# Kernel tuning notes

Hardware: AMD Instinct MI355X
Metric: run time of the kernel (lower is better)

## Reference

```python
import jax, jax.numpy as jnp
import numpy as np

B, T, D = 32, 512, 256
F = 256  # duration_predictor_filter_size
K = 3    # kernel size, padding=1
MEL_MAX = 2304
EPS = 1e-5


def _conv1d(x, w, b):
    # x: [B, T, C_in], w: [C_out, C_in, K], 'same'-ish padding=1
    y = jax.lax.conv_general_dilated(
        x.transpose(0, 2, 1), w, window_strides=(1,), padding=[(1, 1)],
        dimension_numbers=("NCH", "OIH", "NCH"))
    return y.transpose(0, 2, 1) + b


def _layernorm(x, g, b):
    mu = jnp.mean(x, axis=-1, keepdims=True)
    var = jnp.mean(jnp.square(x - mu), axis=-1, keepdims=True)
    return (x - mu) * jax.lax.rsqrt(var + EPS) * g + b


def setup_inputs() -> dict:
    key = jax.random.key(0)
    ks = jax.random.split(key, 8)
    x = jax.random.normal(ks[0], (B, T, D), dtype=jnp.float32)
    target = jax.random.randint(ks[1], (B, T), 0, 8, dtype=jnp.int32)
    s = 0.02
    return {
        "x": x,
        "target": target,
        "mel_max_length": MEL_MAX,
        "conv1_w": jax.random.normal(ks[2], (F, D, K), dtype=jnp.float32) * s,
        "conv1_b": jnp.zeros((F,), jnp.float32),
        "ln1_g": jnp.ones((F,), jnp.float32),
        "ln1_b": jnp.zeros((F,), jnp.float32),
        "conv2_w": jax.random.normal(ks[3], (F, F, K), dtype=jnp.float32) * s,
        "conv2_b": jnp.zeros((F,), jnp.float32),
        "ln2_g": jnp.ones((F,), jnp.float32),
        "ln2_b": jnp.zeros((F,), jnp.float32),
        "lin_w": jax.random.normal(ks[4], (1, F), dtype=jnp.float32) * s,
        "lin_b": jnp.zeros((1,), jnp.float32),
    }


def reference(x, target, mel_max_length, conv1_w, conv1_b, ln1_g, ln1_b,
              conv2_w, conv2_b, ln2_g, ln2_b, lin_w, lin_b):
    # Variance_adaptor (duration predictor), eval-mode dropout = identity
    h = jax.nn.relu(_layernorm(_conv1d(x, conv1_w, conv1_b), ln1_g, ln1_b))
    h = jax.nn.relu(_layernorm(_conv1d(h, conv2_w, conv2_b), ln2_g, ln2_b))
    dur_pred = jax.nn.relu(jnp.einsum("btf,of->bto", h, lin_w) + lin_b)[..., 0]  # [B,T]

    # LR: alignment @ x, expressed as the equivalent duration-indexed gather.
    # alignment[b, t_out, j] = 1 iff cumsum(dur)[b,j-1] <= t_out < cumsum(dur)[b,j]
    cum = jnp.cumsum(target, axis=1)                    # [B, T]
    t_out = jnp.arange(mel_max_length, dtype=cum.dtype)  # [T_out]
    idx = jax.vmap(lambda c: jnp.searchsorted(c, t_out, side="right"))(cum)  # [B, T_out]
    valid = (t_out[None, :] < cum[:, -1:]).astype(x.dtype)                   # [B, T_out]
    gathered = jnp.take_along_axis(x, jnp.clip(idx, 0, T - 1)[:, :, None], axis=1)
    output = gathered * valid[:, :, None]                # zeros past total length (pad)
    return output, dur_pred
```

## Files before the change

### kernel.cpp

```cpp
#include <hip/hip_runtime.h>

typedef __attribute__((ext_vector_type(8))) short short8;
typedef __attribute__((ext_vector_type(4))) float floatx4;

typedef __attribute__((address_space(3))) unsigned int lds_u32;
typedef __attribute__((address_space(1))) const unsigned int glb_u32;

static __device__ __forceinline__ unsigned short f2bf(float f) {
    unsigned int u = __float_as_uint(f);
    return (unsigned short)((u + 0x7FFFu + ((u >> 16) & 1u)) >> 16);
}
static __device__ __forceinline__ void cp16(const ushort* g, ushort* l) {
    __builtin_amdgcn_global_load_lds((glb_u32*)g, (lds_u32*)l, 16, 0, 0);
}

__global__ __launch_bounds__(256)
void prep_kernel(const float* __restrict__ x, const int* __restrict__ target,
                 const float* __restrict__ w1, const float* __restrict__ w2,
                 ushort* __restrict__ xb, ushort* __restrict__ h1b,
                 ushort* __restrict__ w1q, ushort* __restrict__ w2q,
                 float* __restrict__ out0)
{
    __shared__ int cum[512], ps[256], sidx[64];
    const int blk = blockIdx.x, tid = threadIdx.x;
    if (blk < 1152) {
        const int b = blk / 36, t0o = (blk % 36) * 64;
        const int v0 = target[b * 512 + 2 * tid];
        const int v1 = target[b * 512 + 2 * tid + 1];
        ps[tid] = v0 + v1;
        __syncthreads();
        for (int off = 1; off < 256; off <<= 1) {
            int t = (tid >= off) ? ps[tid - off] : 0;
            __syncthreads();
            ps[tid] += t;
            __syncthreads();
        }
        const int excl = tid ? ps[tid - 1] : 0;
        cum[2 * tid]     = excl + v0;
        cum[2 * tid + 1] = excl + v0 + v1;
        __syncthreads();
        const int total = cum[511];
        if (tid < 64) {
            int t = t0o + tid;
            int lo = 0, hi = 512;
            while (lo < hi) {
                int mid = (lo + hi) >> 1;
                if (cum[mid] <= t) lo = mid + 1; else hi = mid;
            }
            sidx[tid] = (t < total) ? ((lo < 512) ? lo : 511) : -1;
        }
        __syncthreads();
        const float4* x4 = (const float4*)x;
        float4* o4 = (float4*)out0;
        const int lane6 = tid & 63, g4 = tid >> 6;
        #pragma unroll 4
        for (int rr = 0; rr < 16; ++rr) {
            int r = rr * 4 + g4;
            int idx = sidx[r];
            float4 v = make_float4(0.f, 0.f, 0.f, 0.f);
            if (idx >= 0) v = x4[((size_t)(b * 512 + idx)) * 64 + lane6];
            o4[((size_t)(b * 2304 + t0o + r)) * 64 + lane6] = v;
        }
    } else if (blk < 5264) {
        const int r = (blk - 1152) * 4 + (tid >> 6);
        const int c = (tid & 63) * 4;
        const int b = r / 514, tp = r % 514;
        ushort4 o;
        if (tp >= 1 && tp <= 512) {
            float4 v = *(const float4*)(x + ((size_t)(b * 512 + tp - 1) * 256 + c));
            o.x = f2bf(v.x); o.y = f2bf(v.y); o.z = f2bf(v.z); o.w = f2bf(v.w);
        } else {
            o.x = o.y = o.z = o.w = 0;
            *(ushort4*)(h1b + (size_t)r * 256 + c) = o;
        }
        *(ushort4*)(xb + (size_t)r * 256 + c) = o;
    } else {
        const bool second = blk >= 6032;
        const int e = (blk - (second ? 6032 : 5264)) * 256 + tid;
        const float* w = second ? w2 : w1;
        ushort* wq = second ? w2q : w1q;
        const int f = e / 768, j = e % 768;
        const int c = j & 255, kr = j >> 8;
        const int se = kr * 4 + (c >> 6);
        const int kk = c & 63;
        const int wg = f >> 6, ni = (f >> 4) & 3, colf = f & 15;
        const int kh = kk >> 5, qk = (kk >> 3) & 3, jj = kk & 7;
        wq[(size_t)se * 16384 + wg * 4096 + (ni * 2 + kh) * 512
           + (qk * 16 + colf) * 8 + jj] = f2bf(w[f * 768 + c * 3 + kr]);
    }
}

template<bool IS_CONV2>
__global__ __launch_bounds__(256, 3)
void conv_mfma_kernel(const ushort* __restrict__ src,
                      const ushort* __restrict__ wq,
                      const float* __restrict__ cbias,
                      const float* __restrict__ gamma, const float* __restrict__ beta,
                      const float* __restrict__ lw, const float* __restrict__ lb,
                      ushort* __restrict__ outb,
                      float* __restrict__ durp)
{
    __shared__ ushort As[2][2048];
    __shared__ float sum_s[4][32], sq_s[4][32], mu_s[32], rs_s[32];

    const int tid = threadIdx.x;
    const int w_ = tid >> 6, lane = tid & 63;
    const int q = lane >> 4, col = lane & 15;
    const int b  = blockIdx.x & 31;
    const int t0 = (blockIdx.x >> 5) << 5;
    const int rot = blockIdx.x % 12;

    floatx4 acc[2][4] = {};
    const int arow = tid >> 3, aquad = (tid & 7) ^ (arow & 7);
    const ushort* xbb = src + (size_t)b * 514 * 256;
    const ushort* bptr = wq + (size_t)w_ * 4096 + lane * 8;

    auto se_of = [&](int s) { int v = s + rot; return v >= 12 ? v - 12 : v; };
#define STAGE_A(SE_, BUF_) do {                                                   \
        const int se_ = (SE_);                                                    \
        const int krow_ = se_ >> 2, cbo_ = (se_ & 3) << 6;                        \
        cp16(xbb + (size_t)(t0 + krow_ + arow) * 256 + cbo_ + aquad * 8,          \
             &As[BUF_][0] + w_ * 512);                                            \
    } while (0)

    STAGE_A(se_of(0), 0);
    __syncthreads();

    int cur = 0;
    #pragma unroll
    for (int s = 0; s < 12; ++s) {
        const int nb = cur ^ 1;
        if (s + 1 < 12) STAGE_A(se_of(s + 1), nb);
        const int se = se_of(s);
        short8 bf[4][2], af[2][2];
        #pragma unroll
        for (int ni = 0; ni < 4; ++ni)
            #pragma unroll
            for (int kh = 0; kh < 2; ++kh)
                bf[ni][kh] = *(const short8*)(bptr + (size_t)se * 16384 + (ni * 2 + kh) * 512);
        #pragma unroll
        for (int mi = 0; mi < 2; ++mi)
            #pragma unroll
            for (int kh = 0; kh < 2; ++kh)
                af[mi][kh] = *(const short8*)((const char*)&As[cur][0]
                    + (mi * 16 + col) * 128 + (((kh * 4 + q) ^ (col & 7)) * 16));
        #pragma unroll
        for (int kh = 0; kh < 2; ++kh)
            #pragma unroll
            for (int mi = 0; mi < 2; ++mi)
                #pragma unroll
                for (int ni = 0; ni < 4; ++ni)
                    acc[mi][ni] = __builtin_amdgcn_mfma_f32_16x16x32_bf16(
                        af[mi][kh], bf[ni][kh], acc[mi][ni], 0, 0, 0);
        __syncthreads();
        cur = nb;
    }
#undef STAGE_A

    const int base_c = w_ * 64;
    float cb4[4], gm4[4], bt4[4];
    #pragma unroll
    for (int ni = 0; ni < 4; ++ni) {
        cb4[ni] = cbias[base_c + ni * 16 + col];
        gm4[ni] = gamma[base_c + ni * 16 + col];
        bt4[ni] = beta [base_c + ni * 16 + col];
    }
    float rsum[2][4] = {}, rsq[2][4] = {};
    #pragma unroll
    for (int mi = 0; mi < 2; ++mi)
        #pragma unroll
        for (int ni = 0; ni < 4; ++ni)
            #pragma unroll
            for (int r = 0; r < 4; ++r) {
                float v = acc[mi][ni][r] + cb4[ni];
                acc[mi][ni][r] = v;
                rsum[mi][r] += v;
                rsq [mi][r] += v * v;
            }
    #pragma unroll
    for (int mi = 0; mi < 2; ++mi)
        #pragma unroll
        for (int r = 0; r < 4; ++r) {
            float s = rsum[mi][r], ss = rsq[mi][r];
            #pragma unroll
            for (int d = 8; d > 0; d >>= 1) {
                s  += __shfl_down(s,  d, 16);
                ss += __shfl_down(ss, d, 16);
            }
            if (col == 0) {
                sum_s[w_][mi * 16 + q * 4 + r] = s;
                sq_s [w_][mi * 16 + q * 4 + r] = ss;
            }
        }
    __syncthreads();
    if (tid < 32) {
        float s  = sum_s[0][tid] + sum_s[1][tid] + sum_s[2][tid] + sum_s[3][tid];
        float ss = sq_s [0][tid] + sq_s [1][tid] + sq_s [2][tid] + sq_s [3][tid];
        float mu = s * (1.f / 256.f);
        mu_s[tid] = mu;
        rs_s[tid] = rsqrtf(ss * (1.f / 256.f) - mu * mu + 1e-5f);
    }
    __syncthreads();

    if (!IS_CONV2) {
        #pragma unroll
        for (int mi = 0; mi < 2; ++mi)
            #pragma unroll
            for (int ni = 0; ni < 4; ++ni)
                #pragma unroll
                for (int r = 0; r < 4; ++r) {
                    int row = mi * 16 + q * 4 + r;
                    float v = (acc[mi][ni][r] - mu_s[row]) * rs_s[row] * gm4[ni] + bt4[ni];
                    outb[((size_t)b * 514 + t0 + row + 1) * 256 + base_c + ni * 16 + col]
                        = f2bf(fmaxf(v, 0.f));
                }
    } else {
        float lw4[4];
        #pragma unroll
        for (int ni = 0; ni < 4; ++ni) lw4[ni] = lw[base_c + ni * 16 + col];
        float dsum[2][4] = {};
        #pragma unroll
        for (int mi = 0; mi < 2; ++mi)
            #pragma unroll
            for (int ni = 0; ni < 4; ++ni)
                #pragma unroll
                for (int r = 0; r < 4; ++r) {
                    int row = mi * 16 + q * 4 + r;
                    float v = (acc[mi][ni][r] - mu_s[row]) * rs_s[row] * gm4[ni] + bt4[ni];
                    dsum[mi][r] += fmaxf(v, 0.f) * lw4[ni];
                }
        #pragma unroll
        for (int mi = 0; mi < 2; ++mi)
            #pragma unroll
            for (int r = 0; r < 4; ++r) {
                float s = dsum[mi][r];
                #pragma unroll
                for (int d = 8; d > 0; d >>= 1) s += __shfl_down(s, d, 16);
                if (col == 0) sum_s[w_][mi * 16 + q * 4 + r] = s;
            }
        __syncthreads();
        if (tid < 32)
            durp[b * 512 + t0 + tid] = fmaxf(sum_s[0][tid] + sum_s[1][tid]
                                           + sum_s[2][tid] + sum_s[3][tid] + lb[0], 0.f);
    }
}

extern "C" void kernel_launch(void* const* d_in, const int* in_sizes, int n_in,
                              void* d_out, int out_size, void* d_ws, size_t ws_size,
                              hipStream_t stream) {
    const float* x      = (const float*)d_in[0];
    const int*   target = (const int*)  d_in[1];
    const float* c1w = (const float*)d_in[3];
    const float* c1b = (const float*)d_in[4];
    const float* g1  = (const float*)d_in[5];
    const float* b1  = (const float*)d_in[6];
    const float* c2w = (const float*)d_in[7];
    const float* c2b = (const float*)d_in[8];
    const float* g2  = (const float*)d_in[9];
    const float* b2  = (const float*)d_in[10];
    const float* lw  = (const float*)d_in[11];
    const float* lb  = (const float*)d_in[12];

    const size_t PADEL = (size_t)32 * 514 * 256;
    ushort* xb   = (ushort*)d_ws;
    ushort* h1b  = xb + PADEL;
    ushort* w1q  = h1b + PADEL;
    ushort* w2q  = w1q + 196608;

    float* out0 = (float*)d_out;
    float* durp = out0 + (size_t)32 * 2304 * 256;

    prep_kernel<<<6800, 256, 0, stream>>>(x, target, c1w, c2w, xb, h1b, w1q, w2q, out0);
    conv_mfma_kernel<false><<<512, 256, 0, stream>>>(
        xb, w1q, c1b, g1, b1, nullptr, nullptr, h1b, nullptr);
    conv_mfma_kernel<true><<<512, 256, 0, stream>>>(
        h1b, w2q, c2b, g2, b2, lw, lb, nullptr, durp);
}
```

Measured before the change: 149.6 us.

## Interleave length-regulator gather blocks into the conv kernels

Moves the length-regulator gather (cumsum, searchsorted, row copy to the output) out of the prep kernel and spreads its 1152 blocks across the two conv launches. Each launch interleaves 8 conv blocks with 9 gather blocks per group of 17, so the memory-bound copy runs alongside the MFMA-bound conv work. The aim is to hide the large output write behind compute and shorten the prep kernel. The cost is higher LDS use per conv block for the extra shared arrays, which may lower occupancy, and blocks within one launch now have uneven work.

```diff
diff --git a/kernel.cpp b/kernel.cpp
--- a/kernel.cpp
+++ b/kernel.cpp
@@ -15,16 +15,65 @@
 }
 
 __global__ __launch_bounds__(256)
-void prep_kernel(const float* __restrict__ x, const int* __restrict__ target,
+void prep_kernel(const float* __restrict__ x,
                  const float* __restrict__ w1, const float* __restrict__ w2,
                  ushort* __restrict__ xb, ushort* __restrict__ h1b,
-                 ushort* __restrict__ w1q, ushort* __restrict__ w2q,
-                 float* __restrict__ out0)
+                 ushort* __restrict__ w1q, ushort* __restrict__ w2q)
 {
+    const int blk = blockIdx.x, tid = threadIdx.x;
+    if (blk < 4112) {
+        const int r = blk * 4 + (tid >> 6);
+        const int c = (tid & 63) * 4;
+        const int b = r / 514, tp = r % 514;
+        ushort4 o;
+        if (tp >= 1 && tp <= 512) {
+            float4 v = *(const float4*)(x + ((size_t)(b * 512 + tp - 1) * 256 + c));
+            o.x = f2bf(v.x); o.y = f2bf(v.y); o.z = f2bf(v.z); o.w = f2bf(v.w);
+        } else {
+            o.x = o.y = o.z = o.w = 0;
+            *(ushort4*)(h1b + (size_t)r * 256 + c) = o;
+        }
+        *(ushort4*)(xb + (size_t)r * 256 + c) = o;
+    } else {
+        const bool second = blk >= 4880;
+        const int e = (blk - (second ? 4880 : 4112)) * 256 + tid;
+        const float* w = second ? w2 : w1;
+        ushort* wq = second ? w2q : w1q;
+        const int f = e / 768, j = e % 768;
+        const int c = j & 255, kr = j >> 8;
+        const int se = kr * 4 + (c >> 6);
+        const int kk = c & 63;
+        const int wg = f >> 6, ni = (f >> 4) & 3, colf = f & 15;
+        const int kh = kk >> 5, qk = (kk >> 3) & 3, jj = kk & 7;
+        wq[(size_t)se * 16384 + wg * 4096 + (ni * 2 + kh) * 512
+           + (qk * 16 + colf) * 8 + jj] = f2bf(w[f * 768 + c * 3 + kr]);
+    }
+}
+
+template<bool IS_CONV2>
+__global__ __launch_bounds__(256, 3)
+void conv_mfma_kernel(const ushort* __restrict__ src,
+                      const ushort* __restrict__ wq,
+                      const float* __restrict__ cbias,
+                      const float* __restrict__ gamma, const float* __restrict__ beta,
+                      const float* __restrict__ lw, const float* __restrict__ lb,
+                      ushort* __restrict__ outb,
+                      float* __restrict__ durp,
+                      const float* __restrict__ x,
+                      const int* __restrict__ target,
+                      float* __restrict__ out0,
+                      int gbase)
+{
+    __shared__ ushort As[2][2048];
+    __shared__ float sum_s[4][32], sq_s[4][32], mu_s[32], rs_s[32];
     __shared__ int cum[512], ps[256], sidx[64];
-    const int blk = blockIdx.x, tid = threadIdx.x;
-    if (blk < 1152) {
-        const int b = blk / 36, t0o = (blk % 36) * 64;
+
+    const int tid = threadIdx.x;
+    const int grp = blockIdx.x / 17, rmod = blockIdx.x % 17;
+
+    if (rmod >= 8) {
+        const int bg = gbase + grp * 9 + (rmod - 8);
+        const int b = bg / 36, t0o = (bg % 36) * 64;
         const int v0 = target[b * 512 + 2 * tid];
         const int v1 = target[b * 512 + 2 * tid + 1];
         ps[tid] = v0 + v1;
@@ -61,54 +110,15 @@
             if (idx >= 0) v = x4[((size_t)(b * 512 + idx)) * 64 + lane6];
             o4[((size_t)(b * 2304 + t0o + r)) * 64 + lane6] = v;
         }
-    } else if (blk < 5264) {
-        const int r = (blk - 1152) * 4 + (tid >> 6);
-        const int c = (tid & 63) * 4;
-        const int b = r / 514, tp = r % 514;
-        ushort4 o;
-        if (tp >= 1 && tp <= 512) {
-            float4 v = *(const float4*)(x + ((size_t)(b * 512 + tp - 1) * 256 + c));
-            o.x = f2bf(v.x); o.y = f2bf(v.y); o.z = f2bf(v.z); o.w = f2bf(v.w);
-        } else {
-            o.x = o.y = o.z = o.w = 0;
-            *(ushort4*)(h1b + (size_t)r * 256 + c) = o;
-        }
-        *(ushort4*)(xb + (size_t)r * 256 + c) = o;
-    } else {
-        const bool second = blk >= 6032;
-        const int e = (blk - (second ? 6032 : 5264)) * 256 + tid;
-        const float* w = second ? w2 : w1;
-        ushort* wq = second ? w2q : w1q;
-        const int f = e / 768, j = e % 768;
-        const int c = j & 255, kr = j >> 8;
-        const int se = kr * 4 + (c >> 6);
-        const int kk = c & 63;
-        const int wg = f >> 6, ni = (f >> 4) & 3, colf = f & 15;
-        const int kh = kk >> 5, qk = (kk >> 3) & 3, jj = kk & 7;
-        wq[(size_t)se * 16384 + wg * 4096 + (ni * 2 + kh) * 512
-           + (qk * 16 + colf) * 8 + jj] = f2bf(w[f * 768 + c * 3 + kr]);
-    }
-}
-
-template<bool IS_CONV2>
-__global__ __launch_bounds__(256, 3)
-void conv_mfma_kernel(const ushort* __restrict__ src,
-                      const ushort* __restrict__ wq,
-                      const float* __restrict__ cbias,
-                      const float* __restrict__ gamma, const float* __restrict__ beta,
-                      const float* __restrict__ lw, const float* __restrict__ lb,
-                      ushort* __restrict__ outb,
-                      float* __restrict__ durp)
-{
-    __shared__ ushort As[2][2048];
-    __shared__ float sum_s[4][32], sq_s[4][32], mu_s[32], rs_s[32];
-
-    const int tid = threadIdx.x;
+        return;
+    }
+    const int conv_id = grp * 8 + rmod;
+
     const int w_ = tid >> 6, lane = tid & 63;
     const int q = lane >> 4, col = lane & 15;
-    const int b  = blockIdx.x & 31;
-    const int t0 = (blockIdx.x >> 5) << 5;
-    const int rot = blockIdx.x % 12;
+    const int b  = conv_id & 31;
+    const int t0 = (conv_id >> 5) << 5;
+    const int rot = conv_id % 12;
 
     floatx4 acc[2][4] = {};
     const int arow = tid >> 3, aquad = (tid & 7) ^ (arow & 7);
@@ -270,9 +280,11 @@
     float* out0 = (float*)d_out;
     float* durp = out0 + (size_t)32 * 2304 * 256;
 
-    prep_kernel<<<6800, 256, 0, stream>>>(x, target, c1w, c2w, xb, h1b, w1q, w2q, out0);
-    conv_mfma_kernel<false><<<512, 256, 0, stream>>>(
-        xb, w1q, c1b, g1, b1, nullptr, nullptr, h1b, nullptr);
-    conv_mfma_kernel<true><<<512, 256, 0, stream>>>(
-        h1b, w2q, c2b, g2, b2, lw, lb, nullptr, durp);
-}
+    prep_kernel<<<5648, 256, 0, stream>>>(x, c1w, c2w, xb, h1b, w1q, w2q);
+    conv_mfma_kernel<false><<<1088, 256, 0, stream>>>(
+        xb, w1q, c1b, g1, b1, nullptr, nullptr, h1b, nullptr,
+        x, target, out0, 0);
+    conv_mfma_kernel<true><<<1088, 256, 0, stream>>>(
+        h1b, w2q, c2b, g2, b2, lw, lb, nullptr, durp,
+        x, target, out0, 576);
+}
```

Result: no change. 152.0 us (+1.6%).
